# Kernel tuning notes

Hardware: AMD Instinct MI355X
Metric: run time of the kernel (lower is better)

The kernel has to match this reference:

```python
import jax, jax.numpy as jnp
import numpy as np

H, W = 512, 512          # pseudo_image_dims
C = 32                   # feat_channels == MHA embed_dim
NH, HD = 2, 16           # heads, head_dim
B, NL, NR = 2, 50000, 20000
EPS = 1e-5
SCALE = np.float32(1.0 / np.sqrt(HD))

# 3x3 neighbor shifts used by shift_bev_grids (INDEX_SHIFT in source)
INDEX_SHIFT = jnp.array([[0, 0], [-1, 0], [1, 0], [0, 1], [-1, 1], [1, 1], [0, -1], [-1, -1], [1, -1]], dtype=jnp.int32)
# 5x5 shifts used by new_gen_dy_coor (gen_index_shift(2))
SHIFT25 = jnp.array([[i, j] for i in range(-2, 3) for j in range(-2, 3)], dtype=jnp.int32)


def _unique_coords(key, n):
    perm = jax.random.permutation(key, H * W)[:n]
    return jnp.stack([perm // W, perm % W], axis=1).astype(jnp.int32)


def setup_inputs():
    key = jax.random.key(0)
    ks = jax.random.split(key, 8)
    inp = {
        "li_bev_feats": jax.random.normal(ks[0], (B, NL, C), jnp.float32),
        "li_bev_coors": jnp.stack([_unique_coords(jax.random.fold_in(ks[1], b), NL) for b in range(B)]),
        "ra_bev_feats": jax.random.normal(ks[2], (B, NR, C), jnp.float32),
        "ra_bev_coors": jnp.stack([_unique_coords(jax.random.fold_in(ks[3], b), NR) for b in range(B)]),
        "radar_bev_dy": jax.random.bernoulli(ks[4], 0.3, (B, NR)),
    }
    pk = jax.random.split(ks[5], 12)
    w = lambda k, o, i: 0.05 * jax.random.normal(k, (o, i), jnp.float32)
    z = lambda n: jnp.zeros((n,), jnp.float32)
    inp.update(
        ln_li_w=jnp.ones((C,), jnp.float32), ln_li_b=z(C),
        ln_ra_w=jnp.ones((C,), jnp.float32), ln_ra_b=z(C),
        q1_w=w(pk[0], C, C), q1_b=z(C), k1_w=w(pk[1], C, C), k1_b=z(C), v1_w=w(pk[2], C, C), v1_b=z(C),
        q2_w=w(pk[3], C, C), q2_b=z(C), k2_w=w(pk[4], C, C), k2_b=z(C), v2_w=w(pk[5], C, C), v2_b=z(C),
        pos_w=w(pk[6], C, 2), pos_b=z(C),
        a1_in_w=w(pk[7], 3 * C, C), a1_in_b=z(3 * C), a1_out_w=w(pk[8], C, C), a1_out_b=z(C),
        a2_in_w=w(pk[9], 3 * C, C), a2_in_b=z(3 * C), a2_out_w=w(pk[10], C, C), a2_out_b=z(C),
    )
    return inp


def _ln(x, w, b):
    mu = jnp.mean(x, -1, keepdims=True)
    var = jnp.mean(jnp.square(x - mu), -1, keepdims=True)
    return (x - mu) / jnp.sqrt(var + EPS) * w + b


def _grid_of(coors, n):
    # dense coord -> pillar-index lookup table, -1 for empty cells
    return jnp.full((H, W), -1, jnp.int32).at[coors[:, 0], coors[:, 1]].set(jnp.arange(n, dtype=jnp.int32))


def _gather_kv(coors, grid, k_map, v_map, pe9):
    # per pillar: look up the 3x3 shifted neighbors in the OTHER modality's grid
    sh = coors[:, None, :] + INDEX_SHIFT[None]                      # [N,9,2]
    inb = (sh[..., 0] >= 0) & (sh[..., 0] < H) & (sh[..., 1] >= 0) & (sh[..., 1] < W)
    idx = grid[jnp.clip(sh[..., 0], 0, H - 1), jnp.clip(sh[..., 1], 0, W - 1)]
    valid = (inb & (idx >= 0))[..., None]                           # [N,9,1]
    safe = jnp.clip(idx, 0, None)
    k = jnp.where(valid, k_map[safe], 0.0)                          # masked_fill(~cond, 0)
    v = jnp.where(valid, v_map[safe] + pe9[None], 0.0)              # pos-enc added before masking
    return k, v


def _mha(q, k, v, Wi, bi, Wo, bo):
    # torch MultiheadAttention (batch_first, eval -> no dropout); q [N,1,C], k/v [N,9,C]
    n = q.shape[0]
    qp = (q @ Wi[:C].T + bi[:C]).reshape(n, 1, NH, HD)
    kp = (k @ Wi[C:2 * C].T + bi[C:2 * C]).reshape(n, -1, NH, HD)
    vp = (v @ Wi[2 * C:].T + bi[2 * C:]).reshape(n, -1, NH, HD)
    s = jnp.einsum("nqhd,nkhd->nhqk", qp, kp) * SCALE
    a = jax.nn.softmax(s, axis=-1)
    o = jnp.einsum("nhqk,nkhd->nqhd", a, vp).reshape(n, C)
    return o @ Wo.T + bo


def _scatter(coors, feat):
    # PointPillarsScatter: place [N,C] features at their (x,y) cells of a [C,H,W] canvas
    return jnp.zeros((H, W, C), feat.dtype).at[coors[:, 0], coors[:, 1]].set(feat).transpose(2, 0, 1)


def _forward(li_bev_feats, li_bev_coors, ra_bev_feats, ra_bev_coors, radar_bev_dy,
             ln_li_w, ln_li_b, ln_ra_w, ln_ra_b,
             q1_w, q1_b, k1_w, k1_b, v1_w, v1_b,
             q2_w, q2_b, k2_w, k2_b, v2_w, v2_b,
             pos_w, pos_b,
             a1_in_w, a1_in_b, a1_out_w, a1_out_b,
             a2_in_w, a2_in_b, a2_out_w, a2_out_b):
    pe9 = INDEX_SHIFT.astype(jnp.float32) @ pos_w.T + pos_b        # [9,C] positional codes

    def per_sample(li_f, li_c, ra_f, ra_c, ra_dy):
        li_n = _ln(li_f, ln_li_w, ln_li_b)
        ra_n = _ln(ra_f, ln_ra_w, ln_ra_b)
        li_grid = _grid_of(li_c, NL)
        ra_grid = _grid_of(ra_c, NR)
        # new_gen_dy_coor: lidar pillars within a 5x5 (mod dims+1) window of any dynamic radar pillar
        g = jnp.array([H + 1, W + 1], jnp.int32)
        sh = (ra_c[:, None, :] + SHIFT25[None]) % g                # [NR,25,2]
        inb = (sh[..., 0] < H) & (sh[..., 1] < W)
        idx = li_grid[jnp.clip(sh[..., 0], 0, H - 1), jnp.clip(sh[..., 1], 0, W - 1)]
        valid = inb & (idx >= 0) & ra_dy[:, None]
        dy_mask = jnp.zeros(NL + 1, bool).at[jnp.where(valid, idx, NL).reshape(-1)].set(True)[:NL]
        # branch 1: dynamic lidar queries cross-attend to 3x3 radar neighbors
        q1 = li_n @ q1_w.T + q1_b
        k1 = ra_n @ k1_w.T + k1_b
        v1 = ra_n @ v1_w.T + v1_b
        k, v = _gather_kv(li_c, ra_grid, k1, v1, pe9)
        out1 = _mha(q1[:, None, :], k, v, a1_in_w, a1_in_b, a1_out_w, a1_out_b)
        out1 = out1 * dy_mask[:, None].astype(out1.dtype)          # only dy pillars scattered
        img_li = _scatter(li_c, out1)
        # branch 2: radar queries cross-attend to 3x3 lidar neighbors
        q2 = ra_n @ q2_w.T + q2_b
        k2 = li_n @ k2_w.T + k2_b
        v2 = li_n @ v2_w.T + v2_b
        k, v = _gather_kv(ra_c, li_grid, k2, v2, pe9)
        out2 = _mha(q2[:, None, :], k, v, a2_in_w, a2_in_b, a2_out_w, a2_out_b)
        img_ra = _scatter(ra_c, out2)
        return img_li, img_ra

    return jax.vmap(per_sample)(li_bev_feats, li_bev_coors, ra_bev_feats, ra_bev_coors, radar_bev_dy)


def reference(li_bev_feats, li_bev_coors, ra_bev_feats, ra_bev_coors, radar_bev_dy,
              ln_li_w, ln_li_b, ln_ra_w, ln_ra_b,
              q1_w, q1_b, k1_w, k1_b, v1_w, v1_b,
              q2_w, q2_b, k2_w, k2_b, v2_w, v2_b,
              pos_w, pos_b,
              a1_in_w, a1_in_b, a1_out_w, a1_out_b,
              a2_in_w, a2_in_b, a2_out_w, a2_out_b):
    return _forward(li_bev_feats, li_bev_coors, ra_bev_feats, ra_bev_coors, radar_bev_dy,
                    ln_li_w, ln_li_b, ln_ra_w, ln_ra_b,
                    q1_w, q1_b, k1_w, k1_b, v1_w, v1_b,
                    q2_w, q2_b, k2_w, k2_b, v2_w, v2_b,
                    pos_w, pos_b,
                    a1_in_w, a1_in_b, a1_out_w, a1_out_b,
                    a2_in_w, a2_in_b, a2_out_w, a2_out_b)
```

## Files before the change

### kernel.cpp

```cpp
#include <hip/hip_runtime.h>
#include <stdint.h>

constexpr int Hh = 512, Ww = 512;
constexpr int C  = 32;
constexpr int B  = 2;
constexpr int NL = 50000;
constexpr int NR = 20000;
constexpr float EPS = 1e-5f;
constexpr float SCALE = 0.25f;

constexpr int CB_MATS = 0;
constexpr int CB_CVEC = 6144;
constexpr int CB_PE1  = 6336;
constexpr int CB_PE2  = 6624;
constexpr int CB_INV  = 6912;
constexpr int CB_TOT  = 7040;

__device__ __constant__ int DX9[9] = {0,-1,1,0,-1,1,0,-1,1};
__device__ __constant__ int DY9[9] = {0,0,0,1,1,1,-1,-1,-1};

__global__ void build_grids_k(const int* __restrict__ li_c, const int* __restrict__ ra_c,
                              int* __restrict__ li_grid, int* __restrict__ ra_grid) {
    int b = blockIdx.y;
    int i = blockIdx.x * blockDim.x + threadIdx.x;
    if (i < NL) {
        int x = li_c[((size_t)b * NL + i) * 2 + 0];
        int y = li_c[((size_t)b * NL + i) * 2 + 1];
        li_grid[(size_t)b * Hh * Ww + x * Ww + y] = i;
    } else if (i < NL + NR) {
        int j = i - NL;
        int x = ra_c[((size_t)b * NR + j) * 2 + 0];
        int y = ra_c[((size_t)b * NR + j) * 2 + 1];
        ra_grid[(size_t)b * Hh * Ww + x * Ww + y] = j;
    }
}

__global__ void const_k(const float* __restrict__ a1w, const float* __restrict__ a1b,
                        const float* __restrict__ a2w, const float* __restrict__ a2b,
                        const float* __restrict__ q1w, const float* __restrict__ q1b,
                        const float* __restrict__ k1w, const float* __restrict__ k1b,
                        const float* __restrict__ v1w, const float* __restrict__ v1b,
                        const float* __restrict__ q2w, const float* __restrict__ q2b,
                        const float* __restrict__ k2w, const float* __restrict__ k2b,
                        const float* __restrict__ v2w, const float* __restrict__ v2b,
                        const float* __restrict__ posw, const float* __restrict__ posb,
                        float* __restrict__ cb) {
    int m = blockIdx.x;
    int t = threadIdx.x;
    if (m < 6) {
        const float* A = (m < 3 ? a1w : a2w) + (m % 3) * C * C;
        const float* Wm;
        switch (m) { case 0: Wm=q1w; break; case 1: Wm=k1w; break; case 2: Wm=v1w; break;
                     case 3: Wm=q2w; break; case 4: Wm=k2w; break; default: Wm=v2w; }
        int r = t >> 5, d = t & 31;
        float s = 0.f;
        #pragma unroll
        for (int c = 0; c < C; ++c) s += A[r * C + c] * Wm[c * C + d];
        cb[CB_MATS + m * 1024 + r * C + d] = s;
        return;
    }
    if (t < 192) {
        int mm = t / 32, r = t & 31;
        const float* A  = (mm < 3 ? a1w : a2w) + (mm % 3) * C * C;
        const float* ab = (mm < 3 ? a1b : a2b) + (mm % 3) * C;
        const float* bv = (mm == 0 ? q1b : mm == 1 ? k1b : mm == 2 ? v1b
                         : mm == 3 ? q2b : mm == 4 ? k2b : v2b);
        float s = ab[r];
        #pragma unroll
        for (int c = 0; c < C; ++c) s += A[r * C + c] * bv[c];
        cb[CB_CVEC + mm * 32 + r] = s;
    } else if (t < 480) {
        int u = t - 192; int j = u >> 5, r = u & 31;
        const float* A = a1w + 2 * C * C;
        float sx = (float)DX9[j], sy = (float)DY9[j];
        float s = 0.f;
        #pragma unroll
        for (int c = 0; c < C; ++c) {
            float pe = posw[c * 2 + 0] * sx + posw[c * 2 + 1] * sy + posb[c];
            s += A[r * C + c] * pe;
        }
        cb[CB_PE1 + j * 32 + r] = s;
    } else if (t < 768) {
        int u = t - 480; int j = u >> 5, r = u & 31;
        const float* A = a2w + 2 * C * C;
        float sx = (float)DX9[j], sy = (float)DY9[j];
        float s = 0.f;
        #pragma unroll
        for (int c = 0; c < C; ++c) {
            float pe = posw[c * 2 + 0] * sx + posw[c * 2 + 1] * sy + posb[c];
            s += A[r * C + c] * pe;
        }
        cb[CB_PE2 + j * 32 + r] = s;
    } else if (t < 896) {
        int u = t - 768; int mm = u >> 5, r = u & 31;
        cb[CB_INV + u] = (mm == 0 ? a1b[32 + r] : mm == 1 ? a1b[64 + r]
                        : mm == 2 ? a2b[32 + r] : a2b[64 + r]);
    }
}

__global__ void ln_proj_k(const float* __restrict__ feats, int n,
                          const float* __restrict__ lnw, const float* __restrict__ lnb,
                          const float* __restrict__ cb, int mq, int mk, int mv,
                          float* __restrict__ qmap, float* __restrict__ kmap,
                          float* __restrict__ vmap) {
    __shared__ float sM[3][1024];
    __shared__ float sc[3][32];
    for (int p = threadIdx.x; p < 1024; p += blockDim.x) {
        sM[0][p] = cb[CB_MATS + mq * 1024 + p];
        sM[1][p] = cb[CB_MATS + mk * 1024 + p];
        sM[2][p] = cb[CB_MATS + mv * 1024 + p];
    }
    if (threadIdx.x < 32) {
        sc[0][threadIdx.x] = cb[CB_CVEC + mq * 32 + threadIdx.x];
        sc[1][threadIdx.x] = cb[CB_CVEC + mk * 32 + threadIdx.x];
        sc[2][threadIdx.x] = cb[CB_CVEC + mv * 32 + threadIdx.x];
    }
    __syncthreads();
    int b = blockIdx.y;
    int i = blockIdx.x * blockDim.x + threadIdx.x;
    if (i >= n) return;

    float x[C];
    const float4* f4 = (const float4*)(feats + ((size_t)b * n + i) * C);
    #pragma unroll
    for (int q = 0; q < 8; ++q) {
        float4 t = f4[q];
        x[4*q] = t.x; x[4*q+1] = t.y; x[4*q+2] = t.z; x[4*q+3] = t.w;
    }
    float mu = 0.f;
    #pragma unroll
    for (int c = 0; c < C; ++c) mu += x[c];
    mu *= (1.0f / C);
    float var = 0.f;
    #pragma unroll
    for (int c = 0; c < C; ++c) { float d = x[c] - mu; var += d * d; }
    var *= (1.0f / C);
    float inv = 1.0f / sqrtf(var + EPS);
    #pragma unroll
    for (int c = 0; c < C; ++c) x[c] = (x[c] - mu) * inv * lnw[c] + lnb[c];

    float* outs[3] = { qmap, kmap, vmap };
    #pragma unroll
    for (int m = 0; m < 3; ++m) {
        float4* o4 = (float4*)(outs[m] + ((size_t)b * n + i) * C);
        #pragma unroll
        for (int rq = 0; rq < 8; ++rq) {
            float4 t;
            float* tp = &t.x;
            #pragma unroll
            for (int rr = 0; rr < 4; ++rr) {
                int r = rq * 4 + rr;
                float s = sc[m][r];
                #pragma unroll
                for (int d = 0; d < C; ++d) s += sM[m][r * C + d] * x[d];
                tp[rr] = s;
            }
            o4[rq] = t;
        }
    }
}

__global__ void dy_mask_k(const int* __restrict__ ra_coors, const int* __restrict__ ra_dy,
                          const int* __restrict__ li_grid, uint8_t* __restrict__ mask) {
    int b = blockIdx.y;
    int r = blockIdx.x * blockDim.x + threadIdx.x;
    if (r >= NR) return;
    if (ra_dy[(size_t)b * NR + r] == 0) return;
    int x = ra_coors[((size_t)b * NR + r) * 2 + 0];
    int y = ra_coors[((size_t)b * NR + r) * 2 + 1];
    #pragma unroll
    for (int dx = -2; dx <= 2; ++dx) {
        #pragma unroll
        for (int dy = -2; dy <= 2; ++dy) {
            int sx = x + dx; sx = (sx < 0) ? sx + (Hh + 1) : (sx >= Hh + 1 ? sx - (Hh + 1) : sx);
            int sy = y + dy; sy = (sy < 0) ? sy + (Ww + 1) : (sy >= Ww + 1 ? sy - (Ww + 1) : sy);
            if (sx < Hh && sy < Ww) {
                int idx = li_grid[(size_t)b * Hh * Ww + sx * Ww + sy];
                if (idx >= 0) mask[(size_t)b * NL + idx] = 1;
            }
        }
    }
}

__global__ void attn_k(const float* __restrict__ qmap, const float* __restrict__ kmap,
                       const float* __restrict__ vmap, const int* __restrict__ q_coors,
                       const int* __restrict__ kv_grid, const float* __restrict__ cb,
                       int pe_off, int kinv_off, int vinv_off,
                       const float* __restrict__ Wo, const float* __restrict__ bo,
                       const uint8_t* __restrict__ mask, float* __restrict__ feat,
                       int nq, int nkv) {
    __shared__ float sWo[1024];
    __shared__ float sbo[32], skinv[32], svinv[32];
    __shared__ float spe[9 * 32];
    for (int p = threadIdx.x; p < 1024; p += blockDim.x) sWo[p] = Wo[p];
    if (threadIdx.x < 32) {
        sbo[threadIdx.x]   = bo[threadIdx.x];
        skinv[threadIdx.x] = cb[kinv_off + threadIdx.x];
        svinv[threadIdx.x] = cb[vinv_off + threadIdx.x];
    }
    for (int p = threadIdx.x; p < 288; p += blockDim.x) spe[p] = cb[pe_off + p];
    __syncthreads();

    int b = blockIdx.y;
    int i = blockIdx.x * blockDim.x + threadIdx.x;
    if (i >= nq) return;
    float4* o4 = (float4*)(feat + ((size_t)b * nq + i) * C);
    if (mask && !mask[(size_t)b * NL + i]) {
        float4 z = {0.f, 0.f, 0.f, 0.f};
        #pragma unroll
        for (int q = 0; q < 8; ++q) o4[q] = z;
        return;
    }

    int x = q_coors[((size_t)b * nq + i) * 2 + 0];
    int y = q_coors[((size_t)b * nq + i) * 2 + 1];

    int nidx[9];
    #pragma unroll
    for (int j = 0; j < 9; ++j) {
        int sx = x + DX9[j], sy = y + DY9[j];
        nidx[j] = (sx >= 0 && sx < Hh && sy >= 0 && sy < Ww)
                  ? kv_grid[(size_t)b * Hh * Ww + sx * Ww + sy] : -1;
    }

    float qp[C];
    const float4* qp4 = (const float4*)(qmap + ((size_t)b * nq + i) * C);
    #pragma unroll
    for (int q = 0; q < 8; ++q) {
        float4 t = qp4[q];
        qp[4*q] = t.x; qp[4*q+1] = t.y; qp[4*q+2] = t.z; qp[4*q+3] = t.w;
    }

    float sc0[9], sc1[9];
    #pragma unroll
    for (int j = 0; j < 9; ++j) {
        int idx = nidx[j];
        const float* kp = (idx >= 0) ? (kmap + ((size_t)b * nkv + idx) * C) : skinv;
        float s0 = 0.f, s1 = 0.f;
        #pragma unroll
        for (int d = 0; d < 16; ++d) { s0 += qp[d] * kp[d]; s1 += qp[16 + d] * kp[16 + d]; }
        sc0[j] = s0 * SCALE; sc1[j] = s1 * SCALE;
    }
    float m0 = sc0[0], m1 = sc1[0];
    #pragma unroll
    for (int j = 1; j < 9; ++j) { m0 = fmaxf(m0, sc0[j]); m1 = fmaxf(m1, sc1[j]); }
    float sum0 = 0.f, sum1 = 0.f;
    #pragma unroll
    for (int j = 0; j < 9; ++j) {
        sc0[j] = expf(sc0[j] - m0); sum0 += sc0[j];
        sc1[j] = expf(sc1[j] - m1); sum1 += sc1[j];
    }
    float r0 = 1.0f / sum0, r1 = 1.0f / sum1;

    float o[C];
    #pragma unroll
    for (int c = 0; c < C; ++c) o[c] = 0.f;
    #pragma unroll
    for (int j = 0; j < 9; ++j) {
        float a0 = sc0[j] * r0, a1 = sc1[j] * r1;
        int idx = nidx[j];
        if (idx >= 0) {
            const float* vp = vmap + ((size_t)b * nkv + idx) * C;
            #pragma unroll
            for (int d = 0; d < 16; ++d) {
                o[d]      += a0 * (vp[d]      + spe[j * 32 + d]);
                o[16 + d] += a1 * (vp[16 + d] + spe[j * 32 + 16 + d]);
            }
        } else {
            #pragma unroll
            for (int d = 0; d < 16; ++d) {
                o[d]      += a0 * svinv[d];
                o[16 + d] += a1 * svinv[16 + d];
            }
        }
    }

    #pragma unroll
    for (int rq = 0; rq < 8; ++rq) {
        float4 t;
        float* tp = &t.x;
        #pragma unroll
        for (int rr = 0; rr < 4; ++rr) {
            int r = rq * 4 + rr;
            float s = sbo[r];
            #pragma unroll
            for (int c = 0; c < C; ++c) s += sWo[r * C + c] * o[c];
            tp[rr] = s;
        }
        o4[rq] = t;
    }
}

__global__ void canvas_k(const int* __restrict__ li_grid, const int* __restrict__ ra_grid,
                         const float* __restrict__ feat1, const float* __restrict__ feat2,
                         float* __restrict__ out_li, float* __restrict__ out_ra) {
    int b = blockIdx.y;
    int cell = blockIdx.x * blockDim.x + threadIdx.x;
    if (cell >= Hh * Ww) return;
    size_t gidx = (size_t)b * Hh * Ww + cell;
    size_t obase = (size_t)b * C * Hh * Ww + cell;

    int li = li_grid[gidx];
    float v[C];
    if (li >= 0) {
        const float4* f = (const float4*)(feat1 + ((size_t)b * NL + li) * C);
        #pragma unroll
        for (int q = 0; q < 8; ++q) {
            float4 t = f[q];
            v[4*q] = t.x; v[4*q+1] = t.y; v[4*q+2] = t.z; v[4*q+3] = t.w;
        }
    } else {
        #pragma unroll
        for (int c = 0; c < C; ++c) v[c] = 0.f;
    }
    #pragma unroll
    for (int c = 0; c < C; ++c) out_li[obase + (size_t)c * Hh * Ww] = v[c];

    int ra = ra_grid[gidx];
    if (ra >= 0) {
        const float4* f = (const float4*)(feat2 + ((size_t)b * NR + ra) * C);
        #pragma unroll
        for (int q = 0; q < 8; ++q) {
            float4 t = f[q];
            v[4*q] = t.x; v[4*q+1] = t.y; v[4*q+2] = t.z; v[4*q+3] = t.w;
        }
    } else {
        #pragma unroll
        for (int c = 0; c < C; ++c) v[c] = 0.f;
    }
    #pragma unroll
    for (int c = 0; c < C; ++c) out_ra[obase + (size_t)c * Hh * Ww] = v[c];
}

extern "C" void kernel_launch(void* const* d_in, const int* in_sizes, int n_in,
                              void* d_out, int out_size, void* d_ws, size_t ws_size,
                              hipStream_t stream) {
    const float*   li_f  = (const float*)d_in[0];
    const int*     li_c  = (const int*)d_in[1];
    const float*   ra_f  = (const float*)d_in[2];
    const int*     ra_c  = (const int*)d_in[3];
    const int*     ra_dy = (const int*)d_in[4];
    const float* ln_li_w = (const float*)d_in[5];
    const float* ln_li_b = (const float*)d_in[6];
    const float* ln_ra_w = (const float*)d_in[7];
    const float* ln_ra_b = (const float*)d_in[8];
    const float* q1w = (const float*)d_in[9],  *q1b = (const float*)d_in[10];
    const float* k1w = (const float*)d_in[11], *k1b = (const float*)d_in[12];
    const float* v1w = (const float*)d_in[13], *v1b = (const float*)d_in[14];
    const float* q2w = (const float*)d_in[15], *q2b = (const float*)d_in[16];
    const float* k2w = (const float*)d_in[17], *k2b = (const float*)d_in[18];
    const float* v2w = (const float*)d_in[19], *v2b = (const float*)d_in[20];
    const float* posw = (const float*)d_in[21], *posb = (const float*)d_in[22];
    const float* a1iw = (const float*)d_in[23], *a1ib = (const float*)d_in[24];
    const float* a1ow = (const float*)d_in[25], *a1ob = (const float*)d_in[26];
    const float* a2iw = (const float*)d_in[27], *a2ib = (const float*)d_in[28];
    const float* a2ow = (const float*)d_in[29], *a2ob = (const float*)d_in[30];

    char* ws = (char*)d_ws;
    size_t off = 0;
    auto carve = [&](size_t bytes) { void* p = ws + off; off += (bytes + 255) & ~(size_t)255; return p; };
    int*     li_grid = (int*)carve((size_t)B * Hh * Ww * 4);
    int*     ra_grid = (int*)carve((size_t)B * Hh * Ww * 4);
    uint8_t* mask    = (uint8_t*)carve((size_t)B * NL);
    float*   cb      = (float*)carve((size_t)CB_TOT * 4);
    float*   qp1   = (float*)carve((size_t)B * NL * C * 4);
    float*   kp1   = (float*)carve((size_t)B * NR * C * 4);
    float*   vp1   = (float*)carve((size_t)B * NR * C * 4);
    float*   qp2   = (float*)carve((size_t)B * NR * C * 4);
    float*   kp2   = (float*)carve((size_t)B * NL * C * 4);
    float*   vp2   = (float*)carve((size_t)B * NL * C * 4);
    float*   feat1 = (float*)carve((size_t)B * NL * C * 4);
    float*   feat2 = (float*)carve((size_t)B * NR * C * 4);
    (void)ws_size; (void)n_in; (void)in_sizes; (void)out_size;

    float* out_li = (float*)d_out;
    float* out_ra = out_li + (size_t)B * C * Hh * Ww;

    hipMemsetAsync(li_grid, 0xFF, (size_t)2 * B * Hh * Ww * 4, stream);
    hipMemsetAsync(mask, 0, (size_t)B * NL, stream);

    const_k<<<dim3(7), dim3(1024), 0, stream>>>(a1iw, a1ib, a2iw, a2ib,
                                                q1w, q1b, k1w, k1b, v1w, v1b,
                                                q2w, q2b, k2w, k2b, v2w, v2b,
                                                posw, posb, cb);
    build_grids_k<<<dim3((NL + NR + 255) / 256, B), dim3(256), 0, stream>>>(li_c, ra_c, li_grid, ra_grid);

    ln_proj_k<<<dim3((NL + 255) / 256, B), dim3(256), 0, stream>>>(li_f, NL, ln_li_w, ln_li_b,
                                                                   cb, 0, 4, 5, qp1, kp2, vp2);
    ln_proj_k<<<dim3((NR + 255) / 256, B), dim3(256), 0, stream>>>(ra_f, NR, ln_ra_w, ln_ra_b,
                                                                   cb, 3, 1, 2, qp2, kp1, vp1);
    dy_mask_k<<<dim3((NR + 255) / 256, B), dim3(256), 0, stream>>>(ra_c, ra_dy, li_grid, mask);

    attn_k<<<dim3((NL + 255) / 256, B), dim3(256), 0, stream>>>(
        qp1, kp1, vp1, li_c, ra_grid, cb, CB_PE1, CB_INV + 0, CB_INV + 32,
        a1ow, a1ob, mask, feat1, NL, NR);
    attn_k<<<dim3((NR + 255) / 256, B), dim3(256), 0, stream>>>(
        qp2, kp2, vp2, ra_c, li_grid, cb, CB_PE2, CB_INV + 64, CB_INV + 96,
        a2ow, a2ob, nullptr, feat2, NR, NL);

    canvas_k<<<dim3((Hh * Ww + 255) / 256, B), dim3(256), 0, stream>>>(
        li_grid, ra_grid, feat1, feat2, out_li, out_ra);
}
```

Before: 375.2 us.

## Merge setup, projection and attention launches; replace scatter dynamic mask with gather

Grid building and constant folding now run in one setup kernel, and a byte grid marks dynamic radar cells. The lidar and radar projection passes share one launch, as do the two attention branches. The dynamic-neighbourhood mask is no longer scattered by a separate kernel; each lidar query instead checks the 5x5 window in the radar-dynamic grid. Key and value loads are vectorised to float4. This cuts launch count and drops the mask kernel and its memset, at the cost of up to 25 byte reads per lidar query and branch divergence inside the merged kernels.

```diff
diff --git a/kernel.cpp b/kernel.cpp
--- a/kernel.cpp
+++ b/kernel.cpp
@@ -2,6 +2,7 @@
 #include <stdint.h>
 
 constexpr int Hh = 512, Ww = 512;
+constexpr int HW = Hh * Ww;
 constexpr int C  = 32;
 constexpr int B  = 2;
 constexpr int NL = 50000;
@@ -9,6 +10,10 @@
 constexpr float EPS = 1e-5f;
 constexpr float SCALE = 0.25f;
 
+constexpr int GBL = (NL + NR + 255) / 256;
+constexpr int LB  = (NL + 255) / 256;
+constexpr int RB  = (NR + 255) / 256;
+
 constexpr int CB_MATS = 0;
 constexpr int CB_CVEC = 6144;
 constexpr int CB_PE1  = 6336;
@@ -19,23 +24,11 @@
 __device__ __constant__ int DX9[9] = {0,-1,1,0,-1,1,0,-1,1};
 __device__ __constant__ int DY9[9] = {0,0,0,1,1,1,-1,-1,-1};
 
-__global__ void build_grids_k(const int* __restrict__ li_c, const int* __restrict__ ra_c,
-                              int* __restrict__ li_grid, int* __restrict__ ra_grid) {
-    int b = blockIdx.y;
-    int i = blockIdx.x * blockDim.x + threadIdx.x;
-    if (i < NL) {
-        int x = li_c[((size_t)b * NL + i) * 2 + 0];
-        int y = li_c[((size_t)b * NL + i) * 2 + 1];
-        li_grid[(size_t)b * Hh * Ww + x * Ww + y] = i;
-    } else if (i < NL + NR) {
-        int j = i - NL;
-        int x = ra_c[((size_t)b * NR + j) * 2 + 0];
-        int y = ra_c[((size_t)b * NR + j) * 2 + 1];
-        ra_grid[(size_t)b * Hh * Ww + x * Ww + y] = j;
-    }
-}
-
-__global__ void const_k(const float* __restrict__ a1w, const float* __restrict__ a1b,
+__global__ void setup_k(const int* __restrict__ li_c, const int* __restrict__ ra_c,
+                        const int* __restrict__ ra_dy,
+                        int* __restrict__ li_grid, int* __restrict__ ra_grid,
+                        uint8_t* __restrict__ rdy_grid,
+                        const float* __restrict__ a1w, const float* __restrict__ a1b,
                         const float* __restrict__ a2w, const float* __restrict__ a2b,
                         const float* __restrict__ q1w, const float* __restrict__ q1b,
                         const float* __restrict__ k1w, const float* __restrict__ k1b,
@@ -45,64 +38,88 @@
                         const float* __restrict__ v2w, const float* __restrict__ v2b,
                         const float* __restrict__ posw, const float* __restrict__ posb,
                         float* __restrict__ cb) {
-    int m = blockIdx.x;
-    int t = threadIdx.x;
-    if (m < 6) {
+    int bx = blockIdx.x, b = blockIdx.y, t = threadIdx.x;
+    if (bx < GBL) {
+        int i = bx * 256 + t;
+        if (i < NL) {
+            int x = li_c[((size_t)b * NL + i) * 2 + 0];
+            int y = li_c[((size_t)b * NL + i) * 2 + 1];
+            li_grid[(size_t)b * HW + x * Ww + y] = i;
+        } else if (i < NL + NR) {
+            int j = i - NL;
+            int x = ra_c[((size_t)b * NR + j) * 2 + 0];
+            int y = ra_c[((size_t)b * NR + j) * 2 + 1];
+            ra_grid[(size_t)b * HW + x * Ww + y] = j;
+            if (ra_dy[(size_t)b * NR + j] != 0)
+                rdy_grid[(size_t)b * HW + x * Ww + y] = 0;
+        }
+        return;
+    }
+    if (b != 0) return;
+    if (bx < GBL + 6) {
+        int m = bx - GBL;
         const float* A = (m < 3 ? a1w : a2w) + (m % 3) * C * C;
         const float* Wm;
         switch (m) { case 0: Wm=q1w; break; case 1: Wm=k1w; break; case 2: Wm=v1w; break;
                      case 3: Wm=q2w; break; case 4: Wm=k2w; break; default: Wm=v2w; }
-        int r = t >> 5, d = t & 31;
-        float s = 0.f;
-        #pragma unroll
-        for (int c = 0; c < C; ++c) s += A[r * C + c] * Wm[c * C + d];
-        cb[CB_MATS + m * 1024 + r * C + d] = s;
+        for (int p = t; p < 1024; p += 256) {
+            int r = p >> 5, d = p & 31;
+            float s = 0.f;
+            #pragma unroll
+            for (int c = 0; c < C; ++c) s += A[r * C + c] * Wm[c * C + d];
+            cb[CB_MATS + m * 1024 + r * C + d] = s;
+        }
         return;
     }
-    if (t < 192) {
-        int mm = t / 32, r = t & 31;
-        const float* A  = (mm < 3 ? a1w : a2w) + (mm % 3) * C * C;
-        const float* ab = (mm < 3 ? a1b : a2b) + (mm % 3) * C;
-        const float* bv = (mm == 0 ? q1b : mm == 1 ? k1b : mm == 2 ? v1b
-                         : mm == 3 ? q2b : mm == 4 ? k2b : v2b);
-        float s = ab[r];
-        #pragma unroll
-        for (int c = 0; c < C; ++c) s += A[r * C + c] * bv[c];
-        cb[CB_CVEC + mm * 32 + r] = s;
-    } else if (t < 480) {
-        int u = t - 192; int j = u >> 5, r = u & 31;
-        const float* A = a1w + 2 * C * C;
-        float sx = (float)DX9[j], sy = (float)DY9[j];
-        float s = 0.f;
-        #pragma unroll
-        for (int c = 0; c < C; ++c) {
-            float pe = posw[c * 2 + 0] * sx + posw[c * 2 + 1] * sy + posb[c];
-            s += A[r * C + c] * pe;
-        }
-        cb[CB_PE1 + j * 32 + r] = s;
-    } else if (t < 768) {
-        int u = t - 480; int j = u >> 5, r = u & 31;
-        const float* A = a2w + 2 * C * C;
-        float sx = (float)DX9[j], sy = (float)DY9[j];
-        float s = 0.f;
-        #pragma unroll
-        for (int c = 0; c < C; ++c) {
-            float pe = posw[c * 2 + 0] * sx + posw[c * 2 + 1] * sy + posb[c];
-            s += A[r * C + c] * pe;
-        }
-        cb[CB_PE2 + j * 32 + r] = s;
-    } else if (t < 896) {
-        int u = t - 768; int mm = u >> 5, r = u & 31;
-        cb[CB_INV + u] = (mm == 0 ? a1b[32 + r] : mm == 1 ? a1b[64 + r]
-                        : mm == 2 ? a2b[32 + r] : a2b[64 + r]);
+    for (int u = t; u < 896; u += 256) {
+        if (u < 192) {
+            int mm = u / 32, r = u & 31;
+            const float* A  = (mm < 3 ? a1w : a2w) + (mm % 3) * C * C;
+            const float* ab = (mm < 3 ? a1b : a2b) + (mm % 3) * C;
+            const float* bv = (mm == 0 ? q1b : mm == 1 ? k1b : mm == 2 ? v1b
+                             : mm == 3 ? q2b : mm == 4 ? k2b : v2b);
+            float s = ab[r];
+            #pragma unroll
+            for (int c = 0; c < C; ++c) s += A[r * C + c] * bv[c];
+            cb[CB_CVEC + mm * 32 + r] = s;
+        } else if (u < 768) {
+            int w = u - 192;
+            int br = w / 288; int v = w % 288; int j = v >> 5, r = v & 31;
+            const float* A = (br == 0 ? a1w : a2w) + 2 * C * C;
+            float sx = (float)DX9[j], sy = (float)DY9[j];
+            float s = 0.f;
+            #pragma unroll
+            for (int c = 0; c < C; ++c) {
+                float pe = posw[c * 2 + 0] * sx + posw[c * 2 + 1] * sy + posb[c];
+                s += A[r * C + c] * pe;
+            }
+            cb[(br == 0 ? CB_PE1 : CB_PE2) + j * 32 + r] = s;
+        } else {
+            int v = u - 768; int mm = v >> 5, r = v & 31;
+            cb[CB_INV + v] = (mm == 0 ? a1b[32 + r] : mm == 1 ? a1b[64 + r]
+                            : mm == 2 ? a2b[32 + r] : a2b[64 + r]);
+        }
     }
 }
 
-__global__ void ln_proj_k(const float* __restrict__ feats, int n,
-                          const float* __restrict__ lnw, const float* __restrict__ lnb,
-                          const float* __restrict__ cb, int mq, int mk, int mv,
-                          float* __restrict__ qmap, float* __restrict__ kmap,
-                          float* __restrict__ vmap) {
+__global__ void ln_proj_k(const float* __restrict__ li_f, const float* __restrict__ ra_f,
+                          const float* __restrict__ ln_li_w, const float* __restrict__ ln_li_b,
+                          const float* __restrict__ ln_ra_w, const float* __restrict__ ln_ra_b,
+                          const float* __restrict__ cb,
+                          float* __restrict__ qp1, float* __restrict__ kp2, float* __restrict__ vp2,
+                          float* __restrict__ qp2, float* __restrict__ kp1, float* __restrict__ vp1) {
+    bool lidar = (blockIdx.x < LB);
+    int n  = lidar ? NL : NR;
+    int i  = (lidar ? blockIdx.x : blockIdx.x - LB) * 256 + threadIdx.x;
+    int b  = blockIdx.y;
+    int mq = lidar ? 0 : 3, mk = lidar ? 4 : 1, mv = lidar ? 5 : 2;
+    const float* feats = lidar ? li_f : ra_f;
+    const float* lnw = lidar ? ln_li_w : ln_ra_w;
+    const float* lnb = lidar ? ln_li_b : ln_ra_b;
+    float* o0 = lidar ? qp1 : qp2;
+    float* o1 = lidar ? kp2 : kp1;
+    float* o2 = lidar ? vp2 : vp1;
+
     __shared__ float sM[3][1024];
     __shared__ float sc[3][32];
     for (int p = threadIdx.x; p < 1024; p += blockDim.x) {
@@ -116,8 +133,6 @@
         sc[2][threadIdx.x] = cb[CB_CVEC + mv * 32 + threadIdx.x];
     }
     __syncthreads();
-    int b = blockIdx.y;
-    int i = blockIdx.x * blockDim.x + threadIdx.x;
     if (i >= n) return;
 
     float x[C];
@@ -139,7 +154,7 @@
     #pragma unroll
     for (int c = 0; c < C; ++c) x[c] = (x[c] - mu) * inv * lnw[c] + lnb[c];
 
-    float* outs[3] = { qmap, kmap, vmap };
+    float* outs[3] = { o0, o1, o2 };
     #pragma unroll
     for (int m = 0; m < 3; ++m) {
         float4* o4 = (float4*)(outs[m] + ((size_t)b * n + i) * C);
@@ -160,35 +175,32 @@
     }
 }
 
-__global__ void dy_mask_k(const int* __restrict__ ra_coors, const int* __restrict__ ra_dy,
-                          const int* __restrict__ li_grid, uint8_t* __restrict__ mask) {
-    int b = blockIdx.y;
-    int r = blockIdx.x * blockDim.x + threadIdx.x;
-    if (r >= NR) return;
-    if (ra_dy[(size_t)b * NR + r] == 0) return;
-    int x = ra_coors[((size_t)b * NR + r) * 2 + 0];
-    int y = ra_coors[((size_t)b * NR + r) * 2 + 1];
-    #pragma unroll
-    for (int dx = -2; dx <= 2; ++dx) {
-        #pragma unroll
-        for (int dy = -2; dy <= 2; ++dy) {
-            int sx = x + dx; sx = (sx < 0) ? sx + (Hh + 1) : (sx >= Hh + 1 ? sx - (Hh + 1) : sx);
-            int sy = y + dy; sy = (sy < 0) ? sy + (Ww + 1) : (sy >= Ww + 1 ? sy - (Ww + 1) : sy);
-            if (sx < Hh && sy < Ww) {
-                int idx = li_grid[(size_t)b * Hh * Ww + sx * Ww + sy];
-                if (idx >= 0) mask[(size_t)b * NL + idx] = 1;
-            }
-        }
-    }
-}
-
-__global__ void attn_k(const float* __restrict__ qmap, const float* __restrict__ kmap,
-                       const float* __restrict__ vmap, const int* __restrict__ q_coors,
-                       const int* __restrict__ kv_grid, const float* __restrict__ cb,
-                       int pe_off, int kinv_off, int vinv_off,
-                       const float* __restrict__ Wo, const float* __restrict__ bo,
-                       const uint8_t* __restrict__ mask, float* __restrict__ feat,
-                       int nq, int nkv) {
+__global__ void attn_k(const float* __restrict__ qp1, const float* __restrict__ kp1,
+                       const float* __restrict__ vp1, const float* __restrict__ qp2,
+                       const float* __restrict__ kp2, const float* __restrict__ vp2,
+                       const int* __restrict__ li_c, const int* __restrict__ ra_c,
+                       const int* __restrict__ li_grid, const int* __restrict__ ra_grid,
+                       const uint8_t* __restrict__ rdy_grid, const float* __restrict__ cb,
+                       const float* __restrict__ a1ow, const float* __restrict__ a1ob,
+                       const float* __restrict__ a2ow, const float* __restrict__ a2ob,
+                       float* __restrict__ feat1, float* __restrict__ feat2) {
+    bool br1 = (blockIdx.x < LB);
+    int nq  = br1 ? NL : NR;
+    int nkv = br1 ? NR : NL;
+    int i   = (br1 ? blockIdx.x : blockIdx.x - LB) * 256 + threadIdx.x;
+    int b   = blockIdx.y;
+    const float* qmap = br1 ? qp1 : qp2;
+    const float* kmap = br1 ? kp1 : kp2;
+    const float* vmap = br1 ? vp1 : vp2;
+    const int* q_coors  = br1 ? li_c : ra_c;
+    const int* kv_grid  = br1 ? ra_grid : li_grid;
+    const float* Wo = br1 ? a1ow : a2ow;
+    const float* bo = br1 ? a1ob : a2ob;
+    int pe_off   = br1 ? CB_PE1 : CB_PE2;
+    int kinv_off = br1 ? CB_INV + 0  : CB_INV + 64;
+    int vinv_off = br1 ? CB_INV + 32 : CB_INV + 96;
+    float* feat  = br1 ? feat1 : feat2;
+
     __shared__ float sWo[1024];
     __shared__ float sbo[32], skinv[32], svinv[32];
     __shared__ float spe[9 * 32];
@@ -201,26 +213,41 @@
     for (int p = threadIdx.x; p < 288; p += blockDim.x) spe[p] = cb[pe_off + p];
     __syncthreads();
 
-    int b = blockIdx.y;
-    int i = blockIdx.x * blockDim.x + threadIdx.x;
     if (i >= nq) return;
     float4* o4 = (float4*)(feat + ((size_t)b * nq + i) * C);
-    if (mask && !mask[(size_t)b * NL + i]) {
-        float4 z = {0.f, 0.f, 0.f, 0.f};
-        #pragma unroll
-        for (int q = 0; q < 8; ++q) o4[q] = z;
-        return;
-    }
 
     int x = q_coors[((size_t)b * nq + i) * 2 + 0];
     int y = q_coors[((size_t)b * nq + i) * 2 + 1];
+
+    if (br1) {
+        bool dy = false;
+        #pragma unroll
+        for (int dx = -2; dx <= 2 && !dy; ++dx) {
+            int cx = x + dx;
+            cx = (cx < 0) ? cx + 513 : (cx >= 513 ? cx - 513 : cx);
+            if (cx == 512) continue;
+            #pragma unroll
+            for (int dyy = -2; dyy <= 2; ++dyy) {
+                int cy = y + dyy;
+                cy = (cy < 0) ? cy + 513 : (cy >= 513 ? cy - 513 : cy);
+                if (cy == 512) continue;
+                if (rdy_grid[(size_t)b * HW + cx * Ww + cy] == 0) { dy = true; break; }
+            }
+        }
+        if (!dy) {
+            float4 z = {0.f, 0.f, 0.f, 0.f};
+            #pragma unroll
+            for (int q = 0; q < 8; ++q) o4[q] = z;
+            return;
+        }
+    }
 
     int nidx[9];
     #pragma unroll
     for (int j = 0; j < 9; ++j) {
         int sx = x + DX9[j], sy = y + DY9[j];
         nidx[j] = (sx >= 0 && sx < Hh && sy >= 0 && sy < Ww)
-                  ? kv_grid[(size_t)b * Hh * Ww + sx * Ww + sy] : -1;
+                  ? kv_grid[(size_t)b * HW + sx * Ww + sy] : -1;
     }
 
     float qp[C];
@@ -235,10 +262,19 @@
     #pragma unroll
     for (int j = 0; j < 9; ++j) {
         int idx = nidx[j];
-        const float* kp = (idx >= 0) ? (kmap + ((size_t)b * nkv + idx) * C) : skinv;
+        const float4* kp4 = (idx >= 0) ? (const float4*)(kmap + ((size_t)b * nkv + idx) * C)
+                                       : (const float4*)skinv;
         float s0 = 0.f, s1 = 0.f;
         #pragma unroll
-        for (int d = 0; d < 16; ++d) { s0 += qp[d] * kp[d]; s1 += qp[16 + d] * kp[16 + d]; }
+        for (int q = 0; q < 4; ++q) {
+            float4 t = kp4[q];
+            s0 += qp[4*q] * t.x + qp[4*q+1] * t.y + qp[4*q+2] * t.z + qp[4*q+3] * t.w;
+        }
+        #pragma unroll
+        for (int q = 4; q < 8; ++q) {
+            float4 t = kp4[q];
+            s1 += qp[4*q] * t.x + qp[4*q+1] * t.y + qp[4*q+2] * t.z + qp[4*q+3] * t.w;
+        }
         sc0[j] = s0 * SCALE; sc1[j] = s1 * SCALE;
     }
     float m0 = sc0[0], m1 = sc1[0];
@@ -260,11 +296,15 @@
         float a0 = sc0[j] * r0, a1 = sc1[j] * r1;
         int idx = nidx[j];
         if (idx >= 0) {
-            const float* vp = vmap + ((size_t)b * nkv + idx) * C;
-            #pragma unroll
-            for (int d = 0; d < 16; ++d) {
-                o[d]      += a0 * (vp[d]      + spe[j * 32 + d]);
-                o[16 + d] += a1 * (vp[16 + d] + spe[j * 32 + 16 + d]);
+            const float4* vp4 = (const float4*)(vmap + ((size_t)b * nkv + idx) * C);
+            #pragma unroll
+            for (int q = 0; q < 8; ++q) {
+                float4 t = vp4[q];
+                float a = (q < 4) ? a0 : a1;
+                o[4*q]   += a * (t.x + spe[j * 32 + 4*q]);
+                o[4*q+1] += a * (t.y + spe[j * 32 + 4*q+1]);
+                o[4*q+2] += a * (t.z + spe[j * 32 + 4*q+2]);
+                o[4*q+3] += a * (t.w + spe[j * 32 + 4*q+3]);
             }
         } else {
             #pragma unroll
@@ -296,9 +336,9 @@
                          float* __restrict__ out_li, float* __restrict__ out_ra) {
     int b = blockIdx.y;
     int cell = blockIdx.x * blockDim.x + threadIdx.x;
-    if (cell >= Hh * Ww) return;
-    size_t gidx = (size_t)b * Hh * Ww + cell;
-    size_t obase = (size_t)b * C * Hh * Ww + cell;
+    if (cell >= HW) return;
+    size_t gidx = (size_t)b * HW + cell;
+    size_t obase = (size_t)b * C * HW + cell;
 
     int li = li_grid[gidx];
     float v[C];
@@ -314,7 +354,7 @@
         for (int c = 0; c < C; ++c) v[c] = 0.f;
     }
     #pragma unroll
-    for (int c = 0; c < C; ++c) out_li[obase + (size_t)c * Hh * Ww] = v[c];
+    for (int c = 0; c < C; ++c) out_li[obase + (size_t)c * HW] = v[c];
 
     int ra = ra_grid[gidx];
     if (ra >= 0) {
@@ -329,7 +369,7 @@
         for (int c = 0; c < C; ++c) v[c] = 0.f;
     }
     #pragma unroll
-    for (int c = 0; c < C; ++c) out_ra[obase + (size_t)c * Hh * Ww] = v[c];
+    for (int c = 0; c < C; ++c) out_ra[obase + (size_t)c * HW] = v[c];
 }
 
 extern "C" void kernel_launch(void* const* d_in, const int* in_sizes, int n_in,
@@ -359,10 +399,11 @@
     char* ws = (char*)d_ws;
     size_t off = 0;
     auto carve = [&](size_t bytes) { void* p = ws + off; off += (bytes + 255) & ~(size_t)255; return p; };
-    int*     li_grid = (int*)carve((size_t)B * Hh * Ww * 4);
-    int*     ra_grid = (int*)carve((size_t)B * Hh * Ww * 4);
-    uint8_t* mask    = (uint8_t*)carve((size_t)B * NL);
-    float*   cb      = (float*)carve((size_t)CB_TOT * 4);
+    int*     li_grid  = (int*)carve((size_t)B * HW * 4);
+    int*     ra_grid  = (int*)carve((size_t)B * HW * 4);
+    uint8_t* rdy_grid = (uint8_t*)carve((size_t)B * HW);
+    size_t   init_bytes = off;
+    float*   cb    = (float*)carve((size_t)CB_TOT * 4);
     float*   qp1   = (float*)carve((size_t)B * NL * C * 4);
     float*   kp1   = (float*)carve((size_t)B * NR * C * 4);
     float*   vp1   = (float*)carve((size_t)B * NR * C * 4);
@@ -374,30 +415,23 @@
     (void)ws_size; (void)n_in; (void)in_sizes; (void)out_size;
 
     float* out_li = (float*)d_out;
-    float* out_ra = out_li + (size_t)B * C * Hh * Ww;
-
-    hipMemsetAsync(li_grid, 0xFF, (size_t)2 * B * Hh * Ww * 4, stream);
-    hipMemsetAsync(mask, 0, (size_t)B * NL, stream);
-
-    const_k<<<dim3(7), dim3(1024), 0, stream>>>(a1iw, a1ib, a2iw, a2ib,
-                                                q1w, q1b, k1w, k1b, v1w, v1b,
-                                                q2w, q2b, k2w, k2b, v2w, v2b,
-                                                posw, posb, cb);
-    build_grids_k<<<dim3((NL + NR + 255) / 256, B), dim3(256), 0, stream>>>(li_c, ra_c, li_grid, ra_grid);
-
-    ln_proj_k<<<dim3((NL + 255) / 256, B), dim3(256), 0, stream>>>(li_f, NL, ln_li_w, ln_li_b,
-                                                                   cb, 0, 4, 5, qp1, kp2, vp2);
-    ln_proj_k<<<dim3((NR + 255) / 256, B), dim3(256), 0, stream>>>(ra_f, NR, ln_ra_w, ln_ra_b,
-                                                                   cb, 3, 1, 2, qp2, kp1, vp1);
-    dy_mask_k<<<dim3((NR + 255) / 256, B), dim3(256), 0, stream>>>(ra_c, ra_dy, li_grid, mask);
-
-    attn_k<<<dim3((NL + 255) / 256, B), dim3(256), 0, stream>>>(
-        qp1, kp1, vp1, li_c, ra_grid, cb, CB_PE1, CB_INV + 0, CB_INV + 32,
-        a1ow, a1ob, mask, feat1, NL, NR);
-    attn_k<<<dim3((NR + 255) / 256, B), dim3(256), 0, stream>>>(
-        qp2, kp2, vp2, ra_c, li_grid, cb, CB_PE2, CB_INV + 64, CB_INV + 96,
-        a2ow, a2ob, nullptr, feat2, NR, NL);
-
-    canvas_k<<<dim3((Hh * Ww + 255) / 256, B), dim3(256), 0, stream>>>(
+    float* out_ra = out_li + (size_t)B * C * HW;
+
+    hipMemsetAsync(li_grid, 0xFF, init_bytes, stream);
+
+    setup_k<<<dim3(GBL + 7, B), dim3(256), 0, stream>>>(
+        li_c, ra_c, ra_dy, li_grid, ra_grid, rdy_grid,
+        a1iw, a1ib, a2iw, a2ib, q1w, q1b, k1w, k1b, v1w, v1b,
+        q2w, q2b, k2w, k2b, v2w, v2b, posw, posb, cb);
+
+    ln_proj_k<<<dim3(LB + RB, B), dim3(256), 0, stream>>>(
+        li_f, ra_f, ln_li_w, ln_li_b, ln_ra_w, ln_ra_b, cb,
+        qp1, kp2, vp2, qp2, kp1, vp1);
+
+    attn_k<<<dim3(LB + RB, B), dim3(256), 0, stream>>>(
+        qp1, kp1, vp1, qp2, kp2, vp2, li_c, ra_c, li_grid, ra_grid, rdy_grid, cb,
+        a1ow, a1ob, a2ow, a2ob, feat1, feat2);
+
+    canvas_k<<<dim3((HW + 255) / 256, B), dim3(256), 0, stream>>>(
         li_grid, ra_grid, feat1, feat2, out_li, out_ra);
 }
```

Result: faster. 331.9 us (-11.5%).
